# Kernel optimization log

Measured on AMD Instinct MI355X. Metric: run time of the kernel, lower is better.

The kernel has to match this reference:

```python
import jax, jax.numpy as jnp
import numpy as np

N_NODES = 100000
N_EDGES = 1600000
N_GRAPHS = 64
IN_FEATS = 86  # 10 + |NodeTypes|(3) + |Devices|(5) + 2*2 + 2*32
GCN_H = 64
FC_H = 32
BN_EPS = 1e-5


def setup_inputs() -> dict:
    key = jax.random.key(0)
    ks = jax.random.split(key, 10)
    x = jax.random.normal(ks[0], (N_NODES, IN_FEATS), dtype=jnp.float32)
    edge_src = jax.random.randint(ks[1], (N_EDGES,), 0, N_NODES, dtype=jnp.int32)
    edge_dst = jax.random.randint(ks[2], (N_EDGES,), 0, N_NODES, dtype=jnp.int32)
    graph_ids = jnp.sort(jax.random.randint(ks[3], (N_NODES,), 0, N_GRAPHS, dtype=jnp.int32))
    bn_gamma = jnp.ones((IN_FEATS,), dtype=jnp.float32)
    bn_beta = jnp.zeros((IN_FEATS,), dtype=jnp.float32)
    W1 = jax.random.normal(ks[4], (IN_FEATS, GCN_H), dtype=jnp.float32) * 0.1
    b1 = jnp.zeros((GCN_H,), dtype=jnp.float32)
    W2 = jax.random.normal(ks[5], (GCN_H, GCN_H), dtype=jnp.float32) * 0.1
    b2 = jnp.zeros((GCN_H,), dtype=jnp.float32)
    fc1_w = jax.random.normal(ks[6], (GCN_H, FC_H), dtype=jnp.float32) * 0.1
    fc1_b = jnp.zeros((FC_H,), dtype=jnp.float32)
    fc2_w = jax.random.normal(ks[7], (FC_H, 1), dtype=jnp.float32) * 0.1
    fc2_b = jnp.zeros((1,), dtype=jnp.float32)
    return {"x": x, "edge_src": edge_src, "edge_dst": edge_dst,
            "graph_ids": graph_ids, "num_graphs": N_GRAPHS,
            "bn_gamma": bn_gamma, "bn_beta": bn_beta,
            "W1": W1, "b1": b1, "W2": W2, "b2": b2,
            "fc1_w": fc1_w, "fc1_b": fc1_b, "fc2_w": fc2_w, "fc2_b": fc2_b}


def _gcn_layer(h, edge_src, edge_dst, W, b):
    # DGL copy_src + mean reduce: each node's h is overwritten by the mean of
    # its in-neighbors' h; zero-in-degree nodes keep their old h (UDF reduce
    # is only applied to nodes with non-empty mailboxes).
    n = h.shape[0]
    msg_sum = jax.ops.segment_sum(h[edge_src], edge_dst, num_segments=n)  # [N, d]
    deg = jax.ops.segment_sum(jnp.ones_like(edge_dst, dtype=h.dtype), edge_dst, num_segments=n)
    agg = jnp.where(deg[:, None] > 0, msg_sum / jnp.maximum(deg, 1.0)[:, None], h)
    return jax.nn.relu(agg @ W + b)


def reference(x, edge_src, edge_dst, graph_ids, num_graphs,
              bn_gamma, bn_beta, W1, b1, W2, b2, fc1_w, fc1_b, fc2_w, fc2_b):
    # BatchNorm1d in training mode: batch stats, biased variance.
    mean = jnp.mean(x, axis=0)
    var = jnp.mean(jnp.square(x - mean), axis=0)
    h = (x - mean) * jax.lax.rsqrt(var + BN_EPS) * bn_gamma + bn_beta
    # Two GCN layers (mean message passing + linear + ReLU).
    h = _gcn_layer(h, edge_src, edge_dst, W1, b1)
    h = _gcn_layer(h, edge_src, edge_dst, W2, b2)
    # dgl.mean_nodes over the batched graph: per-graph mean of node features.
    g_sum = jax.ops.segment_sum(h, graph_ids, num_segments=num_graphs)  # [B, d]
    g_cnt = jax.ops.segment_sum(jnp.ones_like(graph_ids, dtype=h.dtype), graph_ids, num_segments=num_graphs)
    hg = g_sum / jnp.maximum(g_cnt, 1.0)[:, None]
    # FC head (no activation between the two linears, matching the source).
    hg = hg @ fc1_w + fc1_b
    hg = hg @ fc2_w + fc2_b
    return jax.nn.sigmoid(hg).squeeze()
```

## Files before the change

### kernel.cpp

```cpp
#include <hip/hip_runtime.h>

#define N_NODES 100000
#define N_EDGES 1600000
#define N_GRAPHS_C 64
#define IN_F 86
#define H 64
#define N_BKT 391
#define SC_EPT 8
#define SC_TILE 2048
#define SC_GRID 782
#define BC_GRID 1024
#define NW_POOL 2048
typedef unsigned short ushort;

__device__ inline float bf2f(ushort u) { return __uint_as_float(((unsigned)u) << 16); }
__device__ inline ushort f2bf(float f) {
    unsigned x = __float_as_uint(f);
    return (ushort)((x + 0x7fffu + ((x >> 16) & 1u)) >> 16);
}

__global__ void bn_count_k(const float* __restrict__ x, const int* __restrict__ dst,
                           float* __restrict__ bnsum, float* __restrict__ bnsq,
                           int* __restrict__ bcnt) {
    __shared__ float s1[IN_F], s2[IN_F];
    __shared__ int hist[N_BKT];
    int tid = threadIdx.x;
    if (tid < IN_F) { s1[tid] = 0.f; s2[tid] = 0.f; }
    for (int i = tid; i < N_BKT; i += 256) hist[i] = 0;
    __syncthreads();
    if (blockIdx.x < SC_GRID) {
        int e0 = blockIdx.x * SC_TILE;
#pragma unroll
        for (int i = 0; i < SC_EPT; i++) {
            int e = e0 + i * 256 + tid;
            if (e < N_EDGES) atomicAdd(&hist[dst[e] >> 8], 1);
        }
    }
    const int NWAVE = BC_GRID * 4;
    const int RPW = (N_NODES + NWAVE - 1) / NWAVE;
    int lane = tid & 63;
    int w = blockIdx.x * 4 + (tid >> 6);
    int r0 = w * RPW;
    int r1 = min(r0 + RPW, N_NODES);
    float sum0 = 0.f, sq0 = 0.f, sum1 = 0.f, sq1 = 0.f;
#pragma unroll 4
    for (int r = r0; r < r1; r++) {
        const float* base = x + (size_t)r * IN_F;
        float v0 = base[lane];
        float v1 = (lane < IN_F - 64) ? base[64 + lane] : 0.f;
        sum0 += v0; sq0 += v0 * v0;
        sum1 += v1; sq1 += v1 * v1;
    }
    atomicAdd(&s1[lane], sum0);
    atomicAdd(&s2[lane], sq0);
    if (lane < IN_F - 64) {
        atomicAdd(&s1[64 + lane], sum1);
        atomicAdd(&s2[64 + lane], sq1);
    }
    __syncthreads();
    if (tid < IN_F) {
        atomicAdd(&bnsum[tid], s1[tid]);
        atomicAdd(&bnsq[tid], s2[tid]);
    }
    if (blockIdx.x < SC_GRID)
        for (int i = tid; i < N_BKT; i += 256) atomicAdd(&bcnt[i], hist[i]);
}

__global__ void scanprep_k(const int* __restrict__ bcnt, int* __restrict__ bstart,
                           int* __restrict__ gcursor,
                           const float* __restrict__ bnsum, const float* __restrict__ bnsq,
                           const float* __restrict__ gamma, const float* __restrict__ beta,
                           const float* __restrict__ W1, const float* __restrict__ b1,
                           float* __restrict__ W1p, float* __restrict__ c1) {
    __shared__ int tmp[512];
    __shared__ float scale[IN_F], shift[IN_F];
    int t = threadIdx.x;
    int v = (t < N_BKT) ? bcnt[t] : 0;
    tmp[t] = v;
    __syncthreads();
    for (int off = 1; off < 512; off <<= 1) {
        int a = (t >= off) ? tmp[t - off] : 0;
        __syncthreads();
        tmp[t] += a;
        __syncthreads();
    }
    if (t < N_BKT) { bstart[t] = tmp[t] - v; gcursor[t] = tmp[t] - v; }
    if (t == N_BKT - 1) bstart[N_BKT] = tmp[t];
    if (t < IN_F) {
        float mean = bnsum[t] * (1.0f / N_NODES);
        float var  = bnsq[t] * (1.0f / N_NODES) - mean * mean;
        float sc = gamma[t] * rsqrtf(var + 1e-5f);
        scale[t] = sc;
        shift[t] = beta[t] - mean * sc;
    }
    __syncthreads();
    for (int idx = t; idx < IN_F * H; idx += 512) W1p[idx] = scale[idx / H] * W1[idx];
    if (t < H) {
        float acc = b1[t];
        for (int i = 0; i < IN_F; i++) acc += shift[i] * W1[i * H + t];
        c1[t] = acc;
    }
}

__global__ void bucket_scatter_k(const int* __restrict__ src, const int* __restrict__ dst,
                                 int* __restrict__ gcursor, unsigned* __restrict__ ebkt) {
    __shared__ int hist[N_BKT];
    __shared__ int base[N_BKT];
    int tid = threadIdx.x;
    for (int i = tid; i < N_BKT; i += 256) hist[i] = 0;
    __syncthreads();
    int e0 = blockIdx.x * SC_TILE;
    unsigned pk[SC_EPT];
    int bk[SC_EPT], lo[SC_EPT];
#pragma unroll
    for (int i = 0; i < SC_EPT; i++) {
        int e = e0 + i * 256 + tid;
        if (e < N_EDGES) {
            int d = dst[e];
            pk[i] = ((unsigned)src[e] << 8) | (unsigned)(d & 255);
            bk[i] = d >> 8;
            lo[i] = atomicAdd(&hist[bk[i]], 1);
        }
    }
    __syncthreads();
    for (int i = tid; i < N_BKT; i += 256) base[i] = atomicAdd(&gcursor[i], hist[i]);
    __syncthreads();
#pragma unroll
    for (int i = 0; i < SC_EPT; i++) {
        int e = e0 + i * 256 + tid;
        if (e < N_EDGES) ebkt[base[bk[i]] + lo[i]] = pk[i];
    }
}

__global__ void bucket_fill_k(const unsigned* __restrict__ ebkt, const int* __restrict__ bstart,
                              int* __restrict__ rs, int* __restrict__ csr) {
    __shared__ int deg[256];
    __shared__ int scn[256];
    __shared__ int cur[256];
    int b = blockIdx.x;
    int tid = threadIdx.x;
    int e0 = bstart[b], e1 = bstart[b + 1];
    deg[tid] = 0;
    __syncthreads();
    for (int e = e0 + tid; e < e1; e += 256) atomicAdd(&deg[ebkt[e] & 255u], 1);
    __syncthreads();
    scn[tid] = deg[tid];
    __syncthreads();
    for (int off = 1; off < 256; off <<= 1) {
        int a = (tid >= off) ? scn[tid - off] : 0;
        __syncthreads();
        scn[tid] += a;
        __syncthreads();
    }
    int node = (b << 8) + tid;
    if (node < N_NODES) rs[node] = e0 + scn[tid];
    cur[tid] = e0 + scn[tid] - deg[tid];
    __syncthreads();
    for (int e = e0 + tid; e < e1; e += 256) {
        unsigned p = ebkt[e];
        int pos = atomicAdd(&cur[p & 255u], 1);
        csr[pos] = (int)((p & ~255u) >> 1);
    }
}

__global__ __launch_bounds__(256) void gemm_f32_k(const float* __restrict__ X,
                                                  const float* __restrict__ W,
                                                  const float* __restrict__ bias,
                                                  ushort* __restrict__ Y, int N) {
    const int K = IN_F;
    __shared__ __align__(16) float Xt[IN_F][68];
    __shared__ __align__(16) float Wl[IN_F][64];
    int tid = threadIdx.x;
    int row0 = blockIdx.x * 64;
    for (int i = tid; i < K * 64; i += 256) Wl[i / 64][i % 64] = W[i];
    for (int i = tid; i < 64 * K; i += 256) {
        int r = i / K, c = i % K;
        Xt[c][r] = (row0 + r < N) ? X[(size_t)(row0 + r) * K + c] : 0.f;
    }
    __syncthreads();
    int cg = tid & 15, rg = tid >> 4;
    float4 b4 = *(const float4*)&bias[cg * 4];
    float acc[4][4];
    for (int i = 0; i < 4; i++) { acc[i][0] = b4.x; acc[i][1] = b4.y; acc[i][2] = b4.z; acc[i][3] = b4.w; }
    for (int k = 0; k < K; k++) {
        float4 w = *(const float4*)&Wl[k][cg * 4];
        float4 xv = *(const float4*)&Xt[k][rg * 4];
        acc[0][0] += xv.x * w.x; acc[0][1] += xv.x * w.y; acc[0][2] += xv.x * w.z; acc[0][3] += xv.x * w.w;
        acc[1][0] += xv.y * w.x; acc[1][1] += xv.y * w.y; acc[1][2] += xv.y * w.z; acc[1][3] += xv.y * w.w;
        acc[2][0] += xv.z * w.x; acc[2][1] += xv.z * w.y; acc[2][2] += xv.z * w.z; acc[2][3] += xv.z * w.w;
        acc[3][0] += xv.w * w.x; acc[3][1] += xv.w * w.y; acc[3][2] += xv.w * w.z; acc[3][3] += xv.w * w.w;
    }
    for (int i = 0; i < 4; i++) {
        int gr = row0 + rg * 4 + i;
        if (gr < N) {
            ushort4 o;
            o.x = f2bf(acc[i][0]); o.y = f2bf(acc[i][1]);
            o.z = f2bf(acc[i][2]); o.w = f2bf(acc[i][3]);
            *(ushort4*)&Y[(size_t)gr * 64 + cg * 4] = o;
        }
    }
}

__global__ __launch_bounds__(256) void gemm_bf16_k(const ushort* __restrict__ X,
                                                   const float* __restrict__ W,
                                                   const float* __restrict__ bias,
                                                   ushort* __restrict__ Y, int N) {
    const int K = H;
    __shared__ __align__(16) float Xt[H][68];
    __shared__ __align__(16) float Wl[H][64];
    int tid = threadIdx.x;
    int row0 = blockIdx.x * 64;
    for (int i = tid; i < K * 64; i += 256) Wl[i / 64][i % 64] = W[i];
    for (int i = tid; i < 64 * 16; i += 256) {
        int r = i >> 4, c4 = (i & 15) * 4;
        if (row0 + r < N) {
            ushort4 u = *(const ushort4*)&X[(size_t)(row0 + r) * K + c4];
            Xt[c4 + 0][r] = bf2f(u.x); Xt[c4 + 1][r] = bf2f(u.y);
            Xt[c4 + 2][r] = bf2f(u.z); Xt[c4 + 3][r] = bf2f(u.w);
        } else {
            Xt[c4 + 0][r] = 0.f; Xt[c4 + 1][r] = 0.f;
            Xt[c4 + 2][r] = 0.f; Xt[c4 + 3][r] = 0.f;
        }
    }
    __syncthreads();
    int cg = tid & 15, rg = tid >> 4;
    float4 b4 = *(const float4*)&bias[cg * 4];
    float acc[4][4];
    for (int i = 0; i < 4; i++) { acc[i][0] = b4.x; acc[i][1] = b4.y; acc[i][2] = b4.z; acc[i][3] = b4.w; }
    for (int k = 0; k < K; k++) {
        float4 w = *(const float4*)&Wl[k][cg * 4];
        float4 xv = *(const float4*)&Xt[k][rg * 4];
        acc[0][0] += xv.x * w.x; acc[0][1] += xv.x * w.y; acc[0][2] += xv.x * w.z; acc[0][3] += xv.x * w.w;
        acc[1][0] += xv.y * w.x; acc[1][1] += xv.y * w.y; acc[1][2] += xv.y * w.z; acc[1][3] += xv.y * w.w;
        acc[2][0] += xv.z * w.x; acc[2][1] += xv.z * w.y; acc[2][2] += xv.z * w.z; acc[2][3] += xv.z * w.w;
        acc[3][0] += xv.w * w.x; acc[3][1] += xv.w * w.y; acc[3][2] += xv.w * w.z; acc[3][3] += xv.w * w.w;
    }
    for (int i = 0; i < 4; i++) {
        int gr = row0 + rg * 4 + i;
        if (gr < N) {
            ushort4 o;
            o.x = f2bf(acc[i][0]); o.y = f2bf(acc[i][1]);
            o.z = f2bf(acc[i][2]); o.w = f2bf(acc[i][3]);
            *(ushort4*)&Y[(size_t)gr * 64 + cg * 4] = o;
        }
    }
}

__global__ void gather_k(const ushort* __restrict__ g, const int* __restrict__ rs,
                         const int* __restrict__ csr, ushort* __restrict__ out) {
    int lane = threadIdx.x & 63;
    int n = blockIdx.x * 4 + (threadIdx.x >> 6);
    if (n >= N_NODES) return;
    int start = (n == 0) ? 0 : rs[n - 1];
    int end = rs[n];
    int fl = lane & 15;
    int grp = lane >> 4;
    const char* gL = (const char*)g + (fl << 3);
    float a0 = 0.f, a1 = 0.f, a2 = 0.f, a3 = 0.f;
    float b0 = 0.f, b1 = 0.f, b2 = 0.f, b3 = 0.f;
    for (int j0 = start; j0 < end; j0 += 64) {
        int cnt = min(64, end - j0);
        int myoff = (lane < cnt) ? csr[j0 + lane] : 0;
        int j = 0;
        for (; j + 8 <= cnt; j += 8) {
            int s0 = __shfl(myoff, j + grp, 64);
            int s1 = __shfl(myoff, j + 4 + grp, 64);
            uint2 u0 = *(const uint2*)(gL + s0);
            uint2 u1 = *(const uint2*)(gL + s1);
            a0 += __uint_as_float(u0.x << 16);
            a1 += __uint_as_float(u0.x & 0xffff0000u);
            a2 += __uint_as_float(u0.y << 16);
            a3 += __uint_as_float(u0.y & 0xffff0000u);
            b0 += __uint_as_float(u1.x << 16);
            b1 += __uint_as_float(u1.x & 0xffff0000u);
            b2 += __uint_as_float(u1.y << 16);
            b3 += __uint_as_float(u1.y & 0xffff0000u);
        }
        for (; j < cnt; j += 4) {
            int idx = j + grp;
            int s = __shfl(myoff, (idx < cnt) ? idx : (cnt - 1), 64);
            uint2 u = *(const uint2*)(gL + s);
            if (idx < cnt) {
                a0 += __uint_as_float(u.x << 16);
                a1 += __uint_as_float(u.x & 0xffff0000u);
                a2 += __uint_as_float(u.y << 16);
                a3 += __uint_as_float(u.y & 0xffff0000u);
            }
        }
    }
    float v0 = a0 + b0, v1 = a1 + b1, v2 = a2 + b2, v3 = a3 + b3;
    v0 += __shfl_xor(v0, 16, 64); v0 += __shfl_xor(v0, 32, 64);
    v1 += __shfl_xor(v1, 16, 64); v1 += __shfl_xor(v1, 32, 64);
    v2 += __shfl_xor(v2, 16, 64); v2 += __shfl_xor(v2, 32, 64);
    v3 += __shfl_xor(v3, 16, 64); v3 += __shfl_xor(v3, 32, 64);
    if (grp == 0) {
        int d = end - start;
        float r0, r1, r2, r3;
        if (d > 0) {
            float inv = 1.0f / (float)d;
            r0 = v0 * inv; r1 = v1 * inv; r2 = v2 * inv; r3 = v3 * inv;
        } else {
            uint2 u = *(const uint2*)((const char*)g + (size_t)n * 128 + (fl << 3));
            r0 = __uint_as_float(u.x << 16);
            r1 = __uint_as_float(u.x & 0xffff0000u);
            r2 = __uint_as_float(u.y << 16);
            r3 = __uint_as_float(u.y & 0xffff0000u);
        }
        ushort4 o;
        o.x = f2bf(fmaxf(r0, 0.f)); o.y = f2bf(fmaxf(r1, 0.f));
        o.z = f2bf(fmaxf(r2, 0.f)); o.w = f2bf(fmaxf(r3, 0.f));
        *(ushort4*)((char*)out + (size_t)n * 128 + (fl << 3)) = o;
    }
}

__global__ void pool_k(const ushort* __restrict__ h, const int* __restrict__ gid,
                       float* __restrict__ gsum, int* __restrict__ gcnt) {
    int lane = threadIdx.x & 63;
    int wpb = blockDim.x >> 6;
    int gw = blockIdx.x * wpb + (threadIdx.x >> 6);
    const int chunk = (N_NODES + NW_POOL - 1) / NW_POOL;
    int n0 = gw * chunk;
    if (n0 >= N_NODES) return;
    int n1 = min(n0 + chunk, N_NODES);
    float acc = 0.f;
    int cur = gid[n0], cnt = 0;
    for (int n = n0; n < n1; n++) {
        int g = gid[n];
        if (g != cur) {
            atomicAdd(&gsum[cur * H + lane], acc);
            if (lane == 0) atomicAdd(&gcnt[cur], cnt);
            cur = g; acc = 0.f; cnt = 0;
        }
        acc += bf2f(h[(size_t)n * H + lane]);
        cnt++;
    }
    atomicAdd(&gsum[cur * H + lane], acc);
    if (lane == 0) atomicAdd(&gcnt[cur], cnt);
}

__global__ void head_k(const float* __restrict__ gsum, const int* __restrict__ gcnt,
                       const float* __restrict__ fc1w, const float* __restrict__ fc1b,
                       const float* __restrict__ fc2w, const float* __restrict__ fc2b,
                       float* __restrict__ out) {
    __shared__ float w1[H * 32];
    __shared__ float w2[32], bb1[32];
    int b = threadIdx.x;
    for (int i = b; i < H * 32; i += 64) w1[i] = fc1w[i];
    if (b < 32) { w2[b] = fc2w[b]; bb1[b] = fc1b[b]; }
    __syncthreads();
    if (b >= N_GRAPHS_C) return;
    float hg[H];
    float inv = 1.0f / fmaxf((float)gcnt[b], 1.0f);
    for (int k = 0; k < H; k++) hg[k] = gsum[b * H + k] * inv;
    float z = fc2b[0];
    for (int j = 0; j < 32; j++) {
        float t = bb1[j];
        for (int k = 0; k < H; k++) t += hg[k] * w1[k * 32 + j];
        z += t * w2[j];
    }
    out[b] = 1.0f / (1.0f + expf(-z));
}

extern "C" void kernel_launch(void* const* d_in, const int* in_sizes, int n_in,
                              void* d_out, int out_size, void* d_ws, size_t ws_size,
                              hipStream_t stream) {
    const float* x        = (const float*)d_in[0];
    const int*   edge_src = (const int*)d_in[1];
    const int*   edge_dst = (const int*)d_in[2];
    const int*   gid      = (const int*)d_in[3];
    const float* bn_gamma = (const float*)d_in[5];
    const float* bn_beta  = (const float*)d_in[6];
    const float* W1       = (const float*)d_in[7];
    const float* b1       = (const float*)d_in[8];
    const float* W2       = (const float*)d_in[9];
    const float* b2       = (const float*)d_in[10];
    const float* fc1w     = (const float*)d_in[11];
    const float* fc1b     = (const float*)d_in[12];
    const float* fc2w     = (const float*)d_in[13];
    const float* fc2b     = (const float*)d_in[14];
    float* out = (float*)d_out;

    char* ws = (char*)d_ws;
    size_t off = 0;
    auto alloc = [&](size_t bytes) { void* p = ws + off; off += (bytes + 255) & ~(size_t)255; return p; };
    const size_t ZW = IN_F + IN_F + N_BKT + N_GRAPHS_C * H + N_GRAPHS_C;
    float* zreg  = (float*)alloc(ZW * sizeof(float));
    float* bnsum = zreg;
    float* bnsq  = bnsum + IN_F;
    int*   bcnt  = (int*)(bnsq + IN_F);
    float* gsum  = (float*)(bcnt + N_BKT);
    int*   gcnt  = (int*)(gsum + N_GRAPHS_C * H);
    float* W1p     = (float*)alloc(IN_F * H * sizeof(float));
    float* c1      = (float*)alloc(H * sizeof(float));
    int*   bstart  = (int*)alloc((N_BKT + 1) * sizeof(int));
    int*   gcursor = (int*)alloc(N_BKT * sizeof(int));
    int*   rs      = (int*)alloc(N_NODES * sizeof(int));
    int*   csr     = (int*)alloc((size_t)N_EDGES * sizeof(int));
    ushort* gbuf   = (ushort*)alloc((size_t)N_NODES * H * sizeof(ushort));
    ushort* h1     = (ushort*)alloc((size_t)N_NODES * H * sizeof(ushort));
    unsigned* ebkt = (unsigned*)gbuf;

    hipMemsetAsync(zreg, 0, ZW * sizeof(float), stream);

    bn_count_k<<<BC_GRID, 256, 0, stream>>>(x, edge_dst, bnsum, bnsq, bcnt);
    scanprep_k<<<1, 512, 0, stream>>>(bcnt, bstart, gcursor, bnsum, bnsq,
                                      bn_gamma, bn_beta, W1, b1, W1p, c1);
    bucket_scatter_k<<<SC_GRID, 256, 0, stream>>>(edge_src, edge_dst, gcursor, ebkt);
    bucket_fill_k<<<N_BKT, 256, 0, stream>>>(ebkt, bstart, rs, csr);

    gemm_f32_k<<<(N_NODES + 63) / 64, 256, 0, stream>>>(x, W1p, c1, gbuf, N_NODES);
    gather_k<<<(N_NODES + 3) / 4, 256, 0, stream>>>(gbuf, rs, csr, h1);

    gemm_bf16_k<<<(N_NODES + 63) / 64, 256, 0, stream>>>(h1, W2, b2, gbuf, N_NODES);
    gather_k<<<(N_NODES + 3) / 4, 256, 0, stream>>>(gbuf, rs, csr, h1);

    pool_k<<<NW_POOL / 4, 256, 0, stream>>>(h1, gid, gsum, gcnt);
    head_k<<<1, 64, 0, stream>>>(gsum, gcnt, fc1w, fc1b, fc2w, fc2b, out);
}
```

Baseline: 384.4 us.

## Reorder layer 2 as aggregate-then-GEMM and fuse graph pooling into GEMM

The second GCN layer now gathers and averages neighbour features first, then runs the 64x64 GEMM with ReLU. The GEMM epilogue reduces rows per graph in shared memory and atomically adds the sums into the pooled buffer. This removes the separate pool kernel and the write and re-read of the layer-2 output. It relies on aggregation commuting with the linear map, which holds for mean aggregation. GEMM shared-memory tiles are also stored as bf16 to halve LDS usage, which adds a rounding of the BN-folded inputs to bf16.

New measurement: 360.2 us. 6.3% less time.

```diff
diff --git a/kernel.cpp b/kernel.cpp
--- a/kernel.cpp
+++ b/kernel.cpp
@@ -10,7 +10,6 @@
 #define SC_TILE 2048
 #define SC_GRID 782
 #define BC_GRID 1024
-#define NW_POOL 2048
 typedef unsigned short ushort;
 
 __device__ inline float bf2f(ushort u) { return __uint_as_float(((unsigned)u) << 16); }
@@ -168,14 +167,14 @@
                                                   const float* __restrict__ bias,
                                                   ushort* __restrict__ Y, int N) {
     const int K = IN_F;
-    __shared__ __align__(16) float Xt[IN_F][68];
+    __shared__ __align__(16) ushort Xt[IN_F][72];
     __shared__ __align__(16) float Wl[IN_F][64];
     int tid = threadIdx.x;
     int row0 = blockIdx.x * 64;
     for (int i = tid; i < K * 64; i += 256) Wl[i / 64][i % 64] = W[i];
     for (int i = tid; i < 64 * K; i += 256) {
         int r = i / K, c = i % K;
-        Xt[c][r] = (row0 + r < N) ? X[(size_t)(row0 + r) * K + c] : 0.f;
+        Xt[c][r] = (row0 + r < N) ? f2bf(X[(size_t)(row0 + r) * K + c]) : (ushort)0;
     }
     __syncthreads();
     int cg = tid & 15, rg = tid >> 4;
@@ -184,11 +183,12 @@
     for (int i = 0; i < 4; i++) { acc[i][0] = b4.x; acc[i][1] = b4.y; acc[i][2] = b4.z; acc[i][3] = b4.w; }
     for (int k = 0; k < K; k++) {
         float4 w = *(const float4*)&Wl[k][cg * 4];
-        float4 xv = *(const float4*)&Xt[k][rg * 4];
-        acc[0][0] += xv.x * w.x; acc[0][1] += xv.x * w.y; acc[0][2] += xv.x * w.z; acc[0][3] += xv.x * w.w;
-        acc[1][0] += xv.y * w.x; acc[1][1] += xv.y * w.y; acc[1][2] += xv.y * w.z; acc[1][3] += xv.y * w.w;
-        acc[2][0] += xv.z * w.x; acc[2][1] += xv.z * w.y; acc[2][2] += xv.z * w.z; acc[2][3] += xv.z * w.w;
-        acc[3][0] += xv.w * w.x; acc[3][1] += xv.w * w.y; acc[3][2] += xv.w * w.z; acc[3][3] += xv.w * w.w;
+        ushort4 xu = *(const ushort4*)&Xt[k][rg * 4];
+        float x0 = bf2f(xu.x), x1 = bf2f(xu.y), x2 = bf2f(xu.z), x3 = bf2f(xu.w);
+        acc[0][0] += x0 * w.x; acc[0][1] += x0 * w.y; acc[0][2] += x0 * w.z; acc[0][3] += x0 * w.w;
+        acc[1][0] += x1 * w.x; acc[1][1] += x1 * w.y; acc[1][2] += x1 * w.z; acc[1][3] += x1 * w.w;
+        acc[2][0] += x2 * w.x; acc[2][1] += x2 * w.y; acc[2][2] += x2 * w.z; acc[2][3] += x2 * w.w;
+        acc[3][0] += x3 * w.x; acc[3][1] += x3 * w.y; acc[3][2] += x3 * w.z; acc[3][3] += x3 * w.w;
     }
     for (int i = 0; i < 4; i++) {
         int gr = row0 + rg * 4 + i;
@@ -201,27 +201,28 @@
     }
 }
 
-__global__ __launch_bounds__(256) void gemm_bf16_k(const ushort* __restrict__ X,
+__global__ __launch_bounds__(256) void gemm2pool_k(const ushort* __restrict__ X,
                                                    const float* __restrict__ W,
                                                    const float* __restrict__ bias,
-                                                   ushort* __restrict__ Y, int N) {
+                                                   const int* __restrict__ gid,
+                                                   float* __restrict__ gsum,
+                                                   int* __restrict__ gcnt, int N) {
     const int K = H;
-    __shared__ __align__(16) float Xt[H][68];
+    __shared__ __align__(16) ushort Xt[H][72];
     __shared__ __align__(16) float Wl[H][64];
+    __shared__ int gl[64];
+    __shared__ __align__(16) float red[16][64];
     int tid = threadIdx.x;
     int row0 = blockIdx.x * 64;
     for (int i = tid; i < K * 64; i += 256) Wl[i / 64][i % 64] = W[i];
     for (int i = tid; i < 64 * 16; i += 256) {
         int r = i >> 4, c4 = (i & 15) * 4;
-        if (row0 + r < N) {
-            ushort4 u = *(const ushort4*)&X[(size_t)(row0 + r) * K + c4];
-            Xt[c4 + 0][r] = bf2f(u.x); Xt[c4 + 1][r] = bf2f(u.y);
-            Xt[c4 + 2][r] = bf2f(u.z); Xt[c4 + 3][r] = bf2f(u.w);
-        } else {
-            Xt[c4 + 0][r] = 0.f; Xt[c4 + 1][r] = 0.f;
-            Xt[c4 + 2][r] = 0.f; Xt[c4 + 3][r] = 0.f;
-        }
-    }
+        ushort4 u = (row0 + r < N) ? *(const ushort4*)&X[(size_t)(row0 + r) * K + c4]
+                                   : make_ushort4(0, 0, 0, 0);
+        Xt[c4 + 0][r] = u.x; Xt[c4 + 1][r] = u.y;
+        Xt[c4 + 2][r] = u.z; Xt[c4 + 3][r] = u.w;
+    }
+    if (tid < 64) gl[tid] = (row0 + tid < N) ? gid[row0 + tid] : -1;
     __syncthreads();
     int cg = tid & 15, rg = tid >> 4;
     float4 b4 = *(const float4*)&bias[cg * 4];
@@ -229,20 +230,46 @@
     for (int i = 0; i < 4; i++) { acc[i][0] = b4.x; acc[i][1] = b4.y; acc[i][2] = b4.z; acc[i][3] = b4.w; }
     for (int k = 0; k < K; k++) {
         float4 w = *(const float4*)&Wl[k][cg * 4];
-        float4 xv = *(const float4*)&Xt[k][rg * 4];
-        acc[0][0] += xv.x * w.x; acc[0][1] += xv.x * w.y; acc[0][2] += xv.x * w.z; acc[0][3] += xv.x * w.w;
-        acc[1][0] += xv.y * w.x; acc[1][1] += xv.y * w.y; acc[1][2] += xv.y * w.z; acc[1][3] += xv.y * w.w;
-        acc[2][0] += xv.z * w.x; acc[2][1] += xv.z * w.y; acc[2][2] += xv.z * w.z; acc[2][3] += xv.z * w.w;
-        acc[3][0] += xv.w * w.x; acc[3][1] += xv.w * w.y; acc[3][2] += xv.w * w.z; acc[3][3] += xv.w * w.w;
-    }
-    for (int i = 0; i < 4; i++) {
-        int gr = row0 + rg * 4 + i;
-        if (gr < N) {
-            ushort4 o;
-            o.x = f2bf(acc[i][0]); o.y = f2bf(acc[i][1]);
-            o.z = f2bf(acc[i][2]); o.w = f2bf(acc[i][3]);
-            *(ushort4*)&Y[(size_t)gr * 64 + cg * 4] = o;
-        }
+        ushort4 xu = *(const ushort4*)&Xt[k][rg * 4];
+        float x0 = bf2f(xu.x), x1 = bf2f(xu.y), x2 = bf2f(xu.z), x3 = bf2f(xu.w);
+        acc[0][0] += x0 * w.x; acc[0][1] += x0 * w.y; acc[0][2] += x0 * w.z; acc[0][3] += x0 * w.w;
+        acc[1][0] += x1 * w.x; acc[1][1] += x1 * w.y; acc[1][2] += x1 * w.z; acc[1][3] += x1 * w.w;
+        acc[2][0] += x2 * w.x; acc[2][1] += x2 * w.y; acc[2][2] += x2 * w.z; acc[2][3] += x2 * w.w;
+        acc[3][0] += x3 * w.x; acc[3][1] += x3 * w.y; acc[3][2] += x3 * w.z; acc[3][3] += x3 * w.w;
+    }
+    for (int i = 0; i < 4; i++)
+        for (int j = 0; j < 4; j++) acc[i][j] = fmaxf(acc[i][j], 0.f);
+    int rstart = 0;
+    while (rstart < 64) {
+        int g = gl[rstart];
+        if (g < 0) break;
+        int rend = rstart + 1;
+        while (rend < 64 && gl[rend] == g) rend++;
+        float p0 = 0.f, p1 = 0.f, p2 = 0.f, p3 = 0.f;
+#pragma unroll
+        for (int i = 0; i < 4; i++) {
+            int r = rg * 4 + i;
+            if (r >= rstart && r < rend) { p0 += acc[i][0]; p1 += acc[i][1]; p2 += acc[i][2]; p3 += acc[i][3]; }
+        }
+        *(float4*)&red[rg][cg * 4] = make_float4(p0, p1, p2, p3);
+        __syncthreads();
+        for (int s = 8; s >= 1; s >>= 1) {
+            if (rg < s) {
+                float4 a = *(float4*)&red[rg][cg * 4];
+                float4 b = *(float4*)&red[rg + s][cg * 4];
+                *(float4*)&red[rg][cg * 4] = make_float4(a.x + b.x, a.y + b.y, a.z + b.z, a.w + b.w);
+            }
+            __syncthreads();
+        }
+        if (rg == 0) {
+            atomicAdd(&gsum[g * 64 + cg * 4 + 0], red[0][cg * 4 + 0]);
+            atomicAdd(&gsum[g * 64 + cg * 4 + 1], red[0][cg * 4 + 1]);
+            atomicAdd(&gsum[g * 64 + cg * 4 + 2], red[0][cg * 4 + 2]);
+            atomicAdd(&gsum[g * 64 + cg * 4 + 3], red[0][cg * 4 + 3]);
+        }
+        if (tid == 0) atomicAdd(&gcnt[g], rend - rstart);
+        rstart = rend;
+        __syncthreads();
     }
 }
 
@@ -313,29 +340,70 @@
     }
 }
 
-__global__ void pool_k(const ushort* __restrict__ h, const int* __restrict__ gid,
-                       float* __restrict__ gsum, int* __restrict__ gcnt) {
+__global__ void gather_noact_k(const ushort* __restrict__ g, const int* __restrict__ rs,
+                               const int* __restrict__ csr, ushort* __restrict__ out) {
     int lane = threadIdx.x & 63;
-    int wpb = blockDim.x >> 6;
-    int gw = blockIdx.x * wpb + (threadIdx.x >> 6);
-    const int chunk = (N_NODES + NW_POOL - 1) / NW_POOL;
-    int n0 = gw * chunk;
-    if (n0 >= N_NODES) return;
-    int n1 = min(n0 + chunk, N_NODES);
-    float acc = 0.f;
-    int cur = gid[n0], cnt = 0;
-    for (int n = n0; n < n1; n++) {
-        int g = gid[n];
-        if (g != cur) {
-            atomicAdd(&gsum[cur * H + lane], acc);
-            if (lane == 0) atomicAdd(&gcnt[cur], cnt);
-            cur = g; acc = 0.f; cnt = 0;
-        }
-        acc += bf2f(h[(size_t)n * H + lane]);
-        cnt++;
-    }
-    atomicAdd(&gsum[cur * H + lane], acc);
-    if (lane == 0) atomicAdd(&gcnt[cur], cnt);
+    int n = blockIdx.x * 4 + (threadIdx.x >> 6);
+    if (n >= N_NODES) return;
+    int start = (n == 0) ? 0 : rs[n - 1];
+    int end = rs[n];
+    int fl = lane & 15;
+    int grp = lane >> 4;
+    const char* gL = (const char*)g + (fl << 3);
+    float a0 = 0.f, a1 = 0.f, a2 = 0.f, a3 = 0.f;
+    float b0 = 0.f, b1 = 0.f, b2 = 0.f, b3 = 0.f;
+    for (int j0 = start; j0 < end; j0 += 64) {
+        int cnt = min(64, end - j0);
+        int myoff = (lane < cnt) ? csr[j0 + lane] : 0;
+        int j = 0;
+        for (; j + 8 <= cnt; j += 8) {
+            int s0 = __shfl(myoff, j + grp, 64);
+            int s1 = __shfl(myoff, j + 4 + grp, 64);
+            uint2 u0 = *(const uint2*)(gL + s0);
+            uint2 u1 = *(const uint2*)(gL + s1);
+            a0 += __uint_as_float(u0.x << 16);
+            a1 += __uint_as_float(u0.x & 0xffff0000u);
+            a2 += __uint_as_float(u0.y << 16);
+            a3 += __uint_as_float(u0.y & 0xffff0000u);
+            b0 += __uint_as_float(u1.x << 16);
+            b1 += __uint_as_float(u1.x & 0xffff0000u);
+            b2 += __uint_as_float(u1.y << 16);
+            b3 += __uint_as_float(u1.y & 0xffff0000u);
+        }
+        for (; j < cnt; j += 4) {
+            int idx = j + grp;
+            int s = __shfl(myoff, (idx < cnt) ? idx : (cnt - 1), 64);
+            uint2 u = *(const uint2*)(gL + s);
+            if (idx < cnt) {
+                a0 += __uint_as_float(u.x << 16);
+                a1 += __uint_as_float(u.x & 0xffff0000u);
+                a2 += __uint_as_float(u.y << 16);
+                a3 += __uint_as_float(u.y & 0xffff0000u);
+            }
+        }
+    }
+    float v0 = a0 + b0, v1 = a1 + b1, v2 = a2 + b2, v3 = a3 + b3;
+    v0 += __shfl_xor(v0, 16, 64); v0 += __shfl_xor(v0, 32, 64);
+    v1 += __shfl_xor(v1, 16, 64); v1 += __shfl_xor(v1, 32, 64);
+    v2 += __shfl_xor(v2, 16, 64); v2 += __shfl_xor(v2, 32, 64);
+    v3 += __shfl_xor(v3, 16, 64); v3 += __shfl_xor(v3, 32, 64);
+    if (grp == 0) {
+        int d = end - start;
+        float r0, r1, r2, r3;
+        if (d > 0) {
+            float inv = 1.0f / (float)d;
+            r0 = v0 * inv; r1 = v1 * inv; r2 = v2 * inv; r3 = v3 * inv;
+        } else {
+            uint2 u = *(const uint2*)((const char*)g + (size_t)n * 128 + (fl << 3));
+            r0 = __uint_as_float(u.x << 16);
+            r1 = __uint_as_float(u.x & 0xffff0000u);
+            r2 = __uint_as_float(u.y << 16);
+            r3 = __uint_as_float(u.y & 0xffff0000u);
+        }
+        ushort4 o;
+        o.x = f2bf(r0); o.y = f2bf(r1); o.z = f2bf(r2); o.w = f2bf(r3);
+        *(ushort4*)((char*)out + (size_t)n * 128 + (fl << 3)) = o;
+    }
 }
 
 __global__ void head_k(const float* __restrict__ gsum, const int* __restrict__ gcnt,
@@ -411,9 +479,8 @@
     gemm_f32_k<<<(N_NODES + 63) / 64, 256, 0, stream>>>(x, W1p, c1, gbuf, N_NODES);
     gather_k<<<(N_NODES + 3) / 4, 256, 0, stream>>>(gbuf, rs, csr, h1);
 
-    gemm_bf16_k<<<(N_NODES + 63) / 64, 256, 0, stream>>>(h1, W2, b2, gbuf, N_NODES);
-    gather_k<<<(N_NODES + 3) / 4, 256, 0, stream>>>(gbuf, rs, csr, h1);
-
-    pool_k<<<NW_POOL / 4, 256, 0, stream>>>(h1, gid, gsum, gcnt);
+    gather_noact_k<<<(N_NODES + 3) / 4, 256, 0, stream>>>(h1, rs, csr, gbuf);
+    gemm2pool_k<<<(N_NODES + 63) / 64, 256, 0, stream>>>(gbuf, W2, b2, gid, gsum, gcnt, N_NODES);
+
     head_k<<<1, 64, 0, stream>>>(gsum, gcnt, fc1w, fc1b, fc2w, fc2b, out);
 }
```
